# Performance work log

Hardware: AMD Instinct MI355X
Metric: run time of the kernel (lower is better)

Reference implementation:

```python
import jax, jax.numpy as jnp
import numpy as np
from jax import lax

M_SLOTS = 8192      # memory rows
N_DIM = 4096        # memory width; == FVS*FVS
FVS = 64            # function_vector_size
PLEN = 64           # max_program_length (== FVS so program->key fc is consistent)
CDIM = 256          # controller_dim
NIN, NOUT = 512, 512
STEPS = 8           # program length (number of program_i steps)
EPS = 1e-8


def setup_inputs() -> dict:
    key = jax.random.key(0)
    ks = jax.random.split(key, 15)
    s = 0.05
    stdev = 1.0 / np.sqrt(N_DIM + M_SLOTS)  # matches initalize_state uniform init
    return {
        "x": jax.random.normal(ks[0], (1, NIN), jnp.float32),
        "program": jax.random.normal(ks[1], (1, STEPS, PLEN), jnp.float32),
        "memory0": jax.random.uniform(ks[2], (M_SLOTS, N_DIM), jnp.float32, -stdev, stdev),
        "input_embedding": jax.random.normal(ks[3], (NIN, FVS), jnp.float32) * s,
        "output_embedding": jax.random.normal(ks[4], (FVS, NOUT), jnp.float32) * s,
        "Wc": jax.random.normal(ks[5], (CDIM, FVS + PLEN), jnp.float32) * s,
        "bc": jnp.zeros((CDIM,), jnp.float32),
        "Wk": jax.random.normal(ks[6], (N_DIM, CDIM), jnp.float32) * s,
        "bk": jnp.zeros((N_DIM,), jnp.float32),
        "We": jax.random.normal(ks[7], (N_DIM, CDIM), jnp.float32) * s,
        "be": jnp.zeros((N_DIM,), jnp.float32),
        "Wa": jax.random.normal(ks[8], (N_DIM, CDIM), jnp.float32) * s,
        "ba": jnp.zeros((N_DIM,), jnp.float32),
        "Wrk": jax.random.normal(ks[9], (N_DIM, PLEN), jnp.float32) * s,
        "brk": jnp.zeros((N_DIM,), jnp.float32),
    }


def _cosine_address(mem, k):
    # mem: [M, N], k: [N] -> softmax over M of cosine similarity (content addressing)
    sim = mem @ k  # [M]
    denom = jnp.sqrt(jnp.sum(mem * mem, axis=1)) * jnp.sqrt(jnp.sum(k * k)) + EPS
    return jax.nn.softmax(sim / denom)  # [M]


def _ntm_forward(x, program, memory0, input_embedding, output_embedding,
                 Wc, bc, Wk, bk, We, be, Wa, ba, Wrk, brk):
    X = x @ input_embedding  # [1, FVS]

    def step(carry, prog_t):
        Xc, mem = carry  # Xc: [1, FVS], mem: [M, N]
        # Controller: sigmoid(Linear(concat(X, program_i)))
        c = jax.nn.sigmoid(jnp.concatenate([Xc[0], prog_t]) @ Wc.T + bc)  # [CDIM]
        # Write head: key / erase / add from controller state, content addressing
        k = jnp.tanh(c @ Wk.T + bk)           # [N]
        e = jax.nn.sigmoid(c @ We.T + be)     # [N]
        a = jnp.tanh(c @ Wa.T + ba)           # [N]
        ww = _cosine_address(mem, k)          # [M]
        mem = mem * (1.0 - ww[:, None] * e[None, :]) + ww[:, None] * a[None, :]
        # Read head: key from program vector, content addressing on updated memory
        kr = jnp.tanh(prog_t @ Wrk.T + brk)   # [N]
        wr = _cosine_address(mem, kr)         # [M]
        read = wr @ mem                       # [N] == last_read
        # Executioner: X <- tanh(X @ last_read.view(FVS, FVS))
        Xn = jnp.tanh(Xc @ read.reshape(FVS, FVS))  # [1, FVS]
        return (Xn, mem), None

    (Xf, _memf), _ = lax.scan(step, (X, memory0), program[0])
    return Xf @ output_embedding  # [1, NOUT]


def reference(x, program, memory0, input_embedding, output_embedding,
              Wc, bc, Wk, bk, We, be, Wa, ba, Wrk, brk):
    return _ntm_forward(x, program, memory0, input_embedding, output_embedding,
                        Wc, bc, Wk, bk, We, be, Wa, ba, Wrk, brk)
```

## Files before the change

kernel.cpp:

```cpp
#include <hip/hip_runtime.h>
#include <hip/hip_fp16.h>
#include <math.h>

#define M_SLOTS 8192
#define N_DIM   4096
#define FVS     64
#define PLEN    64
#define CDIM    256
#define NIN     512
#define NOUT    512
#define STEPS   8
#define EPS_F   1e-8f

#define SROWS   16
#define NSB     (M_SLOTS / SROWS)
#define RROWS   32
#define NRB     (M_SLOTS / RROWS)


__device__ inline float wave_sum(float v) {
    for (int off = 32; off; off >>= 1) v += __shfl_down(v, off);
    return v;
}

__device__ inline float blk_sum_256(float v, float* sh) {
    v = wave_sum(v);
    int lane = threadIdx.x & 63, wid = threadIdx.x >> 6;
    if (lane == 0) sh[wid] = v;
    __syncthreads();
    float r = sh[0] + sh[1] + sh[2] + sh[3];
    __syncthreads();
    return r;
}

template<int CTRL>
__device__ inline float dppf(float x) {
    return __builtin_bit_cast(float, __builtin_amdgcn_update_dpp(
        0, __builtin_bit_cast(int, x), CTRL, 0xF, 0xF, true));
}

__device__ inline float group_reduce8_dpp(const float sv[8], int lane) {
    const bool b2 = (lane & 4) != 0;
    const bool b0 = (lane & 1) != 0;
    const bool b1 = (lane & 2) != 0;
    float a0 = (b2 ? sv[4] : sv[0]) + dppf<0x141>(b2 ? sv[0] : sv[4]);
    float a1 = (b2 ? sv[5] : sv[1]) + dppf<0x141>(b2 ? sv[1] : sv[5]);
    float a2 = (b2 ? sv[6] : sv[2]) + dppf<0x141>(b2 ? sv[2] : sv[6]);
    float a3 = (b2 ? sv[7] : sv[3]) + dppf<0x141>(b2 ? sv[3] : sv[7]);
    float c0 = (b0 ? a2 : a0) + dppf<0xB1>(b0 ? a0 : a2);
    float c1 = (b0 ? a3 : a1) + dppf<0xB1>(b0 ? a1 : a3);
    return (b1 ? c1 : c0) + dppf<0x4E>(b1 ? c0 : c1);
}

__device__ inline float4 ldh4(const unsigned short* __restrict__ base, size_t idx4) {
    ushort4 u = ((const ushort4*)base)[idx4];
    return make_float4(__half2float(__ushort_as_half(u.x)),
                       __half2float(__ushort_as_half(u.y)),
                       __half2float(__ushort_as_half(u.z)),
                       __half2float(__ushort_as_half(u.w)));
}

template<int NUP>
__device__ inline void ld_ww8(const float* __restrict__ wwT, int m, float wv[8]) {
    const float4* p = (const float4*)(wwT + (size_t)m * 8);
    if (NUP > 0) {
        float4 w0 = p[0];
        wv[0] = w0.x; wv[1] = w0.y; wv[2] = w0.z; wv[3] = w0.w;
    }
    if (NUP > 4) {
        float4 w1 = p[1];
        wv[4] = w1.x; wv[5] = w1.y; wv[6] = w1.z; wv[7] = w1.w;
    }
}


__global__ __launch_bounds__(256) void k_convert(const float* __restrict__ src,
                                                 unsigned short* __restrict__ dst) {
    size_t i = (size_t)blockIdx.x * 256 + threadIdx.x;
    float4 v = ((const float4*)src)[i];
    ushort4 o;
    o.x = __half_as_ushort(__float2half_rn(v.x));
    o.y = __half_as_ushort(__float2half_rn(v.y));
    o.z = __half_as_ushort(__float2half_rn(v.z));
    o.w = __half_as_ushort(__float2half_rn(v.w));
    ((ushort4*)dst)[i] = o;
}

__global__ void k_init_ctrl(const float* __restrict__ x, const float* __restrict__ emb,
                            const float* __restrict__ prog0,
                            const float* __restrict__ Wc, const float* __restrict__ bc,
                            float* __restrict__ X, float* __restrict__ c) {
    __shared__ float in[FVS + PLEN];
    int tid = threadIdx.x;
    if (tid < FVS) {
        float acc = 0.f;
        for (int i = 0; i < NIN; ++i) acc += x[i] * emb[i * FVS + tid];
        X[tid] = acc;
        in[tid] = acc;
    } else if (tid < FVS + PLEN) {
        in[tid] = prog0[tid - FVS];
    }
    __syncthreads();
    float acc = bc[tid];
    const float* wrow = Wc + tid * (FVS + PLEN);
    #pragma unroll 8
    for (int i = 0; i < FVS + PLEN; ++i) acc += wrow[i] * in[i];
    c[tid] = 1.f / (1.f + expf(-acc));
}

__device__ inline void keys_row(int gw, float4 cv, int lane, const float* __restrict__ prog,
                                const float* __restrict__ Wk, const float* __restrict__ bk,
                                const float* __restrict__ We, const float* __restrict__ be,
                                const float* __restrict__ Wa, const float* __restrict__ ba,
                                const float* __restrict__ Wrk, const float* __restrict__ brk,
                                float* __restrict__ k, float* __restrict__ e,
                                float* __restrict__ a, float* __restrict__ kr,
                                float* __restrict__ ekr, float* __restrict__ ea,
                                float* __restrict__ e2) {
    float4 wv;
    wv = ((const float4*)(Wk + (size_t)gw * CDIM))[lane];
    float sK = wv.x*cv.x + wv.y*cv.y + wv.z*cv.z + wv.w*cv.w;
    wv = ((const float4*)(We + (size_t)gw * CDIM))[lane];
    float sE = wv.x*cv.x + wv.y*cv.y + wv.z*cv.z + wv.w*cv.w;
    wv = ((const float4*)(Wa + (size_t)gw * CDIM))[lane];
    float sA = wv.x*cv.x + wv.y*cv.y + wv.z*cv.z + wv.w*cv.w;
    float sR = Wrk[(size_t)gw * PLEN + lane] * prog[lane];
    sK = wave_sum(sK); sE = wave_sum(sE); sA = wave_sum(sA); sR = wave_sum(sR);
    if (lane == 0) {
        float ev  = 1.f / (1.f + expf(-(sE + be[gw])));
        float av  = tanhf(sA + ba[gw]);
        float krv = tanhf(sR + brk[gw]);
        k[gw]   = tanhf(sK + bk[gw]);
        e[gw]   = ev;
        a[gw]   = av;
        kr[gw]  = krv;
        ekr[gw] = ev * krv;
        ea[gw]  = ev * av;
        e2[gw]  = ev * ev;
    }
}

__global__ __launch_bounds__(256) void k_keys4(
        const float* __restrict__ c, const float* __restrict__ prog,
        const float* __restrict__ Wk, const float* __restrict__ bk,
        const float* __restrict__ We, const float* __restrict__ be,
        const float* __restrict__ Wa, const float* __restrict__ ba,
        const float* __restrict__ Wrk, const float* __restrict__ brk,
        float* __restrict__ k, float* __restrict__ e,
        float* __restrict__ a, float* __restrict__ kr,
        float* __restrict__ ekr, float* __restrict__ ea, float* __restrict__ e2) {
    int lane = threadIdx.x & 63, wid = threadIdx.x >> 6;
    const float4 cv = ((const float4*)c)[lane];
    for (int gw = blockIdx.x * 4 + wid; gw < 4096; gw += 2048)
        keys_row(gw, cv, lane, prog, Wk, bk, We, be, Wa, ba, Wrk, brk,
                 k, e, a, kr, ekr, ea, e2);
}


template<int NUP>
__global__ __launch_bounds__(256) void k_stats(
        const unsigned short* __restrict__ mem0h,
        const float* __restrict__ ehist, const float* __restrict__ ahist,
        const float* __restrict__ wwT,
        const float* __restrict__ kc, const float* __restrict__ krc,
        const float* __restrict__ ekrc, const float* __restrict__ eac,
        const float* __restrict__ e2c,
        float* __restrict__ stat4) {
    const int tid  = threadIdx.x;
    const int cc   = blockIdx.x;
    const int rb   = blockIdx.y;
    const int col4 = cc * 256 + tid;
    const int lane = tid & 63, wid = tid >> 6;
    const int HN   = (NUP > 0) ? NUP : 1;
    float4 eh[HN], ah[HN];
    #pragma unroll
    for (int s = 0; s < NUP; ++s) {
        eh[s] = ((const float4*)(ehist + (size_t)s * N_DIM))[col4];
        ah[s] = ((const float4*)(ahist + (size_t)s * N_DIM))[col4];
    }
    const float4 kk  = ((const float4*)kc)[col4];
    const float4 rr  = ((const float4*)krc)[col4];
    const float4 fkr = ((const float4*)ekrc)[col4];
    const float4 fea = ((const float4*)eac)[col4];
    const float4 fe2 = ((const float4*)e2c)[col4];
    const float4 ce  = ((const float4*)(ehist + (size_t)NUP * N_DIM))[col4];
    const float4 ca  = ((const float4*)(ahist + (size_t)NUP * N_DIM))[col4];

    __shared__ float shc[4][SROWS][64];

    const int stl = (lane & 4) + 2 * (lane & 1) + ((lane & 2) >> 1);

    #pragma unroll
    for (int r = 0; r < SROWS; ++r) {
        const int m = rb * SROWS + r;
        float4 v = ldh4(mem0h, (size_t)m * (N_DIM / 4) + col4);
        float wv[8];
        ld_ww8<NUP>(wwT, m, wv);
        #pragma unroll
        for (int s = 0; s < NUP; ++s) {
            const float w = wv[s];
            v.x = v.x * (1.f - w * eh[s].x) + w * ah[s].x;
            v.y = v.y * (1.f - w * eh[s].y) + w * ah[s].y;
            v.z = v.z * (1.f - w * eh[s].z) + w * ah[s].z;
            v.w = v.w * (1.f - w * eh[s].w) + w * ah[s].w;
        }
        float sv[8] = {0.f, 0.f, 0.f, 0.f, 0.f, 0.f, 0.f, 0.f};
        #define ACC1(vv,kc_,rc_,ekr_,ac_,ea_,ec_,e2_) { \
            float _v = vv; float _v2 = _v * _v; \
            sv[0] += _v * kc_;  sv[1] += _v * rc_;  sv[2] += _v * ekr_; \
            sv[3] += _v * ac_;  sv[4] += _v * ea_;  sv[5] += _v * _v; \
            sv[6] += _v2 * ec_; sv[7] += _v2 * e2_; }
        ACC1(v.x, kk.x, rr.x, fkr.x, ca.x, fea.x, ce.x, fe2.x)
        ACC1(v.y, kk.y, rr.y, fkr.y, ca.y, fea.y, ce.y, fe2.y)
        ACC1(v.z, kk.z, rr.z, fkr.z, ca.z, fea.z, ce.z, fe2.z)
        ACC1(v.w, kk.w, rr.w, fkr.w, ca.w, fea.w, ce.w, fe2.w)
        #undef ACC1
        float g = group_reduce8_dpp(sv, lane);
        shc[wid][r][(lane & 56) + stl] = g;
    }
    __syncthreads();
    if (tid < SROWS * 8) {
        const int r = tid >> 3, st = tid & 7;
        float tot = 0.f;
        #pragma unroll
        for (int w = 0; w < 4; ++w)
            #pragma unroll
            for (int g2 = 0; g2 < 8; ++g2)
                tot += shc[w][r][g2 * 8 + st];
        stat4[(size_t)(cc * 8 + st) * M_SLOTS + rb * SROWS + r] = tot;
    }
}

#define ST4(st, m) (stat4[(size_t)(st) * M_SLOTS + (m)] \
                  + stat4[(size_t)((st) + 8) * M_SLOTS + (m)] \
                  + stat4[(size_t)((st) + 16) * M_SLOTS + (m)] \
                  + stat4[(size_t)((st) + 24) * M_SLOTS + (m)])

__global__ __launch_bounds__(256) void k_addrA(
        const float* __restrict__ kc, const float* __restrict__ stat4,
        float* __restrict__ exp1, float* __restrict__ n2sav,
        float* __restrict__ psum1) {
    __shared__ float sh4[4];
    const int tid = threadIdx.x, b = blockIdx.x;
    float a0 = 0.f;
    for (int i = tid; i < N_DIM; i += 256) { float kv = kc[i]; a0 += kv * kv; }
    float d0 = blk_sum_256(a0, sh4);
    float knorm = sqrtf(d0);
    float ls = 0.f;
    #pragma unroll
    for (int j = 0; j < 2; ++j) {
        int m = b * 512 + j * 256 + tid;
        float sim = ST4(0, m);
        float n2  = ST4(5, m);
        float v = sim / (sqrtf(n2) * knorm + EPS_F);
        float ex = expf(v);
        exp1[m] = ex;
        n2sav[m] = n2;
        ls += ex;
    }
    float tot = blk_sum_256(ls, sh4);
    if (tid == 0) psum1[b] = tot;
}

template<int NHIST>
__global__ __launch_bounds__(256) void k_read(
        const unsigned short* __restrict__ mem0h,
        const float* __restrict__ ehist, const float* __restrict__ ahist,
        float* __restrict__ wwT,
        const float* __restrict__ krc,
        const float* __restrict__ exp1, const float* __restrict__ n2sav,
        const float* __restrict__ psum1, const float* __restrict__ stat4,
        float* __restrict__ psum2,
        float* __restrict__ partial) {
    const int tid  = threadIdx.x;
    const int cc   = blockIdx.x;
    const int rb   = blockIdx.y;
    const int col4 = cc * 256 + tid;

    __shared__ float sh4[4];
    __shared__ float w1s[RROWS];
    __shared__ float wrs[RROWS];

    const float* ac = ahist + (size_t)NHIST * N_DIM;
    float a1 = 0.f, a2 = 0.f, a3 = 0.f;
    for (int i = tid; i < N_DIM; i += 256) {
        float rv = krc[i], av = ac[i];
        a1 += rv * rv; a2 += av * rv; a3 += av * av;
    }
    float d1 = blk_sum_256(a1, sh4);
    float d2 = blk_sum_256(a2, sh4);
    float d3 = blk_sum_256(a3, sh4);
    float krnorm = sqrtf(d1);

    float s1 = 0.f;
    #pragma unroll
    for (int i = 0; i < 16; ++i) s1 += psum1[i];
    const float inv1 = 1.f / s1;

    if (tid < RROWS) {
        const int m = rb * RROWS + tid;
        float w1 = exp1[m] * inv1;
        w1s[tid] = w1;
        float skr  = ST4(1, m);
        float sekr = ST4(2, m);
        float sa_  = ST4(3, m);
        float sea_ = ST4(4, m);
        float qe_  = ST4(6, m);
        float qe2_ = ST4(7, m);
        float sim2 = skr - w1 * sekr + w1 * d2;
        float n2n  = n2sav[m] - 2.f*w1*qe_ + w1*w1*qe2_
                   + 2.f*w1*sa_ - 2.f*w1*w1*sea_ + w1*w1*d3;
        float v2 = sim2 / (sqrtf(n2n) * krnorm + EPS_F);
        wrs[tid] = expf(v2);
        if (cc == 0) wwT[(size_t)m * 8 + NHIST] = w1;
    }
    __syncthreads();
    if (cc == 0 && tid == 0) {
        float s = 0.f;
        #pragma unroll
        for (int r = 0; r < RROWS; ++r) s += wrs[r];
        psum2[rb] = s;
    }

    const int HN = (NHIST > 0) ? NHIST : 1;
    float4 eh[HN], ah[HN];
    #pragma unroll
    for (int s = 0; s < NHIST; ++s) {
        eh[s] = ((const float4*)(ehist + (size_t)s * N_DIM))[col4];
        ah[s] = ((const float4*)(ahist + (size_t)s * N_DIM))[col4];
    }
    const float4 ce = ((const float4*)(ehist + (size_t)NHIST * N_DIM))[col4];
    const float4 ca = ((const float4*)(ahist + (size_t)NHIST * N_DIM))[col4];

    float4 acc = make_float4(0.f, 0.f, 0.f, 0.f);
    for (int r = 0; r < RROWS; ++r) {
        const int m = rb * RROWS + r;
        float4 v = ldh4(mem0h, (size_t)m * (N_DIM / 4) + col4);
        float wv[8];
        ld_ww8<NHIST>(wwT, m, wv);
        #pragma unroll
        for (int s = 0; s < NHIST; ++s) {
            const float w = wv[s];
            v.x = v.x * (1.f - w * eh[s].x) + w * ah[s].x;
            v.y = v.y * (1.f - w * eh[s].y) + w * ah[s].y;
            v.z = v.z * (1.f - w * eh[s].z) + w * ah[s].z;
            v.w = v.w * (1.f - w * eh[s].w) + w * ah[s].w;
        }
        {
            const float w1 = w1s[r];
            v.x = v.x * (1.f - w1 * ce.x) + w1 * ca.x;
            v.y = v.y * (1.f - w1 * ce.y) + w1 * ca.y;
            v.z = v.z * (1.f - w1 * ce.z) + w1 * ca.z;
            v.w = v.w * (1.f - w1 * ce.w) + w1 * ca.w;
        }
        const float w2 = wrs[r];
        acc.x += w2 * v.x; acc.y += w2 * v.y; acc.z += w2 * v.z; acc.w += w2 * v.w;
    }
    ((float4*)partial)[(size_t)rb * (N_DIM / 4) + col4] = acc;
}

__global__ void k_read_reduce(const float* __restrict__ partial,
                              const float* __restrict__ psum2,
                              float* __restrict__ red) {
    __shared__ float sh4[4];
    __shared__ float gsh[4][64];
    float p = psum2[threadIdx.x];
    float tot = blk_sum_256(p, sh4);
    float inv2 = 1.f / tot;
    int l = threadIdx.x & 63;
    int q = threadIdx.x >> 6;
    int c = blockIdx.x * 64 + l;
    float acc = 0.f;
    #pragma unroll 8
    for (int r = q * (NRB / 4); r < (q + 1) * (NRB / 4); ++r)
        acc += partial[(size_t)r * N_DIM + c];
    gsh[q][l] = acc;
    __syncthreads();
    if (threadIdx.x < 64)
        red[blockIdx.x * 64 + threadIdx.x] = inv2 *
            (gsh[0][threadIdx.x] + gsh[1][threadIdx.x] +
             gsh[2][threadIdx.x] + gsh[3][threadIdx.x]);
}

__global__ __launch_bounds__(256) void k_exec_keys(
        const float* __restrict__ Xold, float* __restrict__ Xnew,
        const float* __restrict__ red, const float* __restrict__ prog_next,
        const float* __restrict__ Wc, const float* __restrict__ bc,
        const float* __restrict__ Wk, const float* __restrict__ bk,
        const float* __restrict__ We, const float* __restrict__ be,
        const float* __restrict__ Wa, const float* __restrict__ ba,
        const float* __restrict__ Wrk, const float* __restrict__ brk,
        float* __restrict__ k, float* __restrict__ e,
        float* __restrict__ a, float* __restrict__ kr,
        float* __restrict__ ekr, float* __restrict__ ea, float* __restrict__ e2) {
    __shared__ float xo[FVS];
    __shared__ float xs[FVS];
    __shared__ float cc[CDIM];
    int tid = threadIdx.x, lane = tid & 63, wid = tid >> 6;
    if (tid < FVS) xo[tid] = Xold[tid];
    __syncthreads();
    if (tid < FVS) {
        float acc = 0.f;
        #pragma unroll
        for (int i = 0; i < FVS; ++i) acc += xo[i] * red[i * FVS + tid];
        float xn = tanhf(acc);
        xs[tid] = xn;
        if (blockIdx.x == 0) Xnew[tid] = xn;
    }
    __syncthreads();
    {
        float acc = bc[tid];
        const float* wrow = Wc + tid * (FVS + PLEN);
        #pragma unroll
        for (int i = 0; i < FVS; ++i) acc += wrow[i] * xs[i];
        #pragma unroll
        for (int i = 0; i < PLEN; ++i) acc += wrow[FVS + i] * prog_next[i];
        cc[tid] = 1.f / (1.f + expf(-acc));
    }
    __syncthreads();
    const float4 cv = ((const float4*)cc)[lane];
    for (int gw = blockIdx.x * 4 + wid; gw < 4096; gw += 2048)
        keys_row(gw, cv, lane, prog_next, Wk, bk, We, be, Wa, ba, Wrk, brk,
                 k, e, a, kr, ekr, ea, e2);
}

__global__ void k_final(const float* __restrict__ Xold, const float* __restrict__ red,
                        const float* __restrict__ out_emb, float* __restrict__ out) {
    __shared__ float xo[FVS];
    __shared__ float xs[FVS];
    int tid = threadIdx.x;
    if (tid < FVS) xo[tid] = Xold[tid];
    __syncthreads();
    if (tid < FVS) {
        float acc = 0.f;
        #pragma unroll
        for (int i = 0; i < FVS; ++i) acc += xo[i] * red[i * FVS + tid];
        xs[tid] = tanhf(acc);
    }
    __syncthreads();
    for (int col = tid; col < NOUT; col += 256) {
        float acc = 0.f;
        #pragma unroll
        for (int i = 0; i < FVS; ++i) acc += xs[i] * out_emb[i * NOUT + col];
        out[col] = acc;
    }
}


extern "C" void kernel_launch(void* const* d_in, const int* in_sizes, int n_in,
                              void* d_out, int out_size, void* d_ws, size_t ws_size,
                              hipStream_t stream) {
    const float* x        = (const float*)d_in[0];
    const float* program  = (const float*)d_in[1];
    const float* memory0  = (const float*)d_in[2];
    const float* in_emb   = (const float*)d_in[3];
    const float* out_emb  = (const float*)d_in[4];
    const float* Wc       = (const float*)d_in[5];
    const float* bc       = (const float*)d_in[6];
    const float* Wk       = (const float*)d_in[7];
    const float* bk       = (const float*)d_in[8];
    const float* We       = (const float*)d_in[9];
    const float* be       = (const float*)d_in[10];
    const float* Wa       = (const float*)d_in[11];
    const float* ba       = (const float*)d_in[12];
    const float* Wrk      = (const float*)d_in[13];
    const float* brk      = (const float*)d_in[14];
    float* out = (float*)d_out;

    float* ws = (float*)d_ws;
    size_t off = 0;
    unsigned short* mem0h = (unsigned short*)(ws + off);
    off += (size_t)M_SLOTS * N_DIM / 2;
    float* ehist   = ws + off; off += (size_t)STEPS * N_DIM;
    float* ahist   = ws + off; off += (size_t)STEPS * N_DIM;
    float* wwT     = ws + off; off += (size_t)M_SLOTS * 8;
    float* kcur    = ws + off; off += N_DIM;
    float* krcur   = ws + off; off += N_DIM;
    float* ekrcur  = ws + off; off += N_DIM;
    float* eacur   = ws + off; off += N_DIM;
    float* e2cur   = ws + off; off += N_DIM;
    float* stat4   = ws + off; off += (size_t)32 * M_SLOTS;
    float* partial = ws + off; off += (size_t)NRB * N_DIM;
    float* exp1    = ws + off; off += M_SLOTS;
    float* n2sav   = ws + off; off += M_SLOTS;
    float* psum1   = ws + off; off += 16;
    float* psum2   = ws + off; off += NRB;
    float* red     = ws + off; off += N_DIM;
    float* Xb0     = ws + off; off += FVS;
    float* Xb1     = ws + off; off += FVS;
    float* c       = ws + off; off += CDIM;

    k_convert<<<(M_SLOTS * (N_DIM / 4)) / 256, 256, 0, stream>>>(memory0, mem0h);
    k_init_ctrl<<<1, 256, 0, stream>>>(x, in_emb, program, Wc, bc, Xb0, c);
    k_keys4<<<512, 256, 0, stream>>>(c, program, Wk, bk, We, be, Wa, ba, Wrk, brk,
                                     kcur, ehist, ahist, krcur, ekrcur, eacur, e2cur);

    const dim3 sgrid(4, NSB), rgrid(4, NRB);

    for (int t = 0; t < STEPS; ++t) {
        switch (t) {
            case 0: k_stats<0><<<sgrid, 256, 0, stream>>>(mem0h, ehist, ahist, wwT,
                        kcur, krcur, ekrcur, eacur, e2cur, stat4); break;
            case 1: k_stats<1><<<sgrid, 256, 0, stream>>>(mem0h, ehist, ahist, wwT,
                        kcur, krcur, ekrcur, eacur, e2cur, stat4); break;
            case 2: k_stats<2><<<sgrid, 256, 0, stream>>>(mem0h, ehist, ahist, wwT,
                        kcur, krcur, ekrcur, eacur, e2cur, stat4); break;
            case 3: k_stats<3><<<sgrid, 256, 0, stream>>>(mem0h, ehist, ahist, wwT,
                        kcur, krcur, ekrcur, eacur, e2cur, stat4); break;
            case 4: k_stats<4><<<sgrid, 256, 0, stream>>>(mem0h, ehist, ahist, wwT,
                        kcur, krcur, ekrcur, eacur, e2cur, stat4); break;
            case 5: k_stats<5><<<sgrid, 256, 0, stream>>>(mem0h, ehist, ahist, wwT,
                        kcur, krcur, ekrcur, eacur, e2cur, stat4); break;
            case 6: k_stats<6><<<sgrid, 256, 0, stream>>>(mem0h, ehist, ahist, wwT,
                        kcur, krcur, ekrcur, eacur, e2cur, stat4); break;
            case 7: k_stats<7><<<sgrid, 256, 0, stream>>>(mem0h, ehist, ahist, wwT,
                        kcur, krcur, ekrcur, eacur, e2cur, stat4); break;
        }

        k_addrA<<<16, 256, 0, stream>>>(kcur, stat4, exp1, n2sav, psum1);

        switch (t) {
            case 0: k_read<0><<<rgrid, 256, 0, stream>>>(mem0h, ehist, ahist, wwT,
                        krcur, exp1, n2sav, psum1, stat4, psum2, partial); break;
            case 1: k_read<1><<<rgrid, 256, 0, stream>>>(mem0h, ehist, ahist, wwT,
                        krcur, exp1, n2sav, psum1, stat4, psum2, partial); break;
            case 2: k_read<2><<<rgrid, 256, 0, stream>>>(mem0h, ehist, ahist, wwT,
                        krcur, exp1, n2sav, psum1, stat4, psum2, partial); break;
            case 3: k_read<3><<<rgrid, 256, 0, stream>>>(mem0h, ehist, ahist, wwT,
                        krcur, exp1, n2sav, psum1, stat4, psum2, partial); break;
            case 4: k_read<4><<<rgrid, 256, 0, stream>>>(mem0h, ehist, ahist, wwT,
                        krcur, exp1, n2sav, psum1, stat4, psum2, partial); break;
            case 5: k_read<5><<<rgrid, 256, 0, stream>>>(mem0h, ehist, ahist, wwT,
                        krcur, exp1, n2sav, psum1, stat4, psum2, partial); break;
            case 6: k_read<6><<<rgrid, 256, 0, stream>>>(mem0h, ehist, ahist, wwT,
                        krcur, exp1, n2sav, psum1, stat4, psum2, partial); break;
            case 7: k_read<7><<<rgrid, 256, 0, stream>>>(mem0h, ehist, ahist, wwT,
                        krcur, exp1, n2sav, psum1, stat4, psum2, partial); break;
        }

        k_read_reduce<<<64, 256, 0, stream>>>(partial, psum2, red);

        const float* Xcur = (t & 1) ? Xb1 : Xb0;
        float*       Xnxt = (t & 1) ? Xb0 : Xb1;
        if (t < STEPS - 1) {
            k_exec_keys<<<512, 256, 0, stream>>>(
                Xcur, Xnxt, red, program + (t + 1) * PLEN,
                Wc, bc, Wk, bk, We, be, Wa, ba, Wrk, brk,
                kcur, ehist + (size_t)(t + 1) * N_DIM,
                ahist + (size_t)(t + 1) * N_DIM, krcur, ekrcur, eacur, e2cur);
        } else {
            k_final<<<1, 256, 0, stream>>>(Xcur, red, out_emb, out);
        }
    }
}
```

Measured before the change: 690.1 us.

## Remap k_stats so each lane owns a memory row and loops over columns

Rewrites the stats kernel so that each lane accumulates all eight statistics for one memory row across a 128-column strip. The per-column vectors are then wave-uniform broadcast loads, which replaces the DPP cross-lane reduction with a small shared-memory reduction over 8 waves. Blocks grow to 512 threads, covering 64 rows by 1024 columns. The cost is that the fp16 memory loads within a wave now stride across 64 different rows, so they are no longer coalesced, and it relies on L1/L2 to reuse cache lines across loop iterations.

```diff
diff --git a/kernel.cpp b/kernel.cpp
--- a/kernel.cpp
+++ b/kernel.cpp
@@ -12,8 +12,6 @@
 #define STEPS   8
 #define EPS_F   1e-8f
 
-#define SROWS   16
-#define NSB     (M_SLOTS / SROWS)
 #define RROWS   32
 #define NRB     (M_SLOTS / RROWS)
 
@@ -31,25 +29,6 @@
     float r = sh[0] + sh[1] + sh[2] + sh[3];
     __syncthreads();
     return r;
-}
-
-template<int CTRL>
-__device__ inline float dppf(float x) {
-    return __builtin_bit_cast(float, __builtin_amdgcn_update_dpp(
-        0, __builtin_bit_cast(int, x), CTRL, 0xF, 0xF, true));
-}
-
-__device__ inline float group_reduce8_dpp(const float sv[8], int lane) {
-    const bool b2 = (lane & 4) != 0;
-    const bool b0 = (lane & 1) != 0;
-    const bool b1 = (lane & 2) != 0;
-    float a0 = (b2 ? sv[4] : sv[0]) + dppf<0x141>(b2 ? sv[0] : sv[4]);
-    float a1 = (b2 ? sv[5] : sv[1]) + dppf<0x141>(b2 ? sv[1] : sv[5]);
-    float a2 = (b2 ? sv[6] : sv[2]) + dppf<0x141>(b2 ? sv[2] : sv[6]);
-    float a3 = (b2 ? sv[7] : sv[3]) + dppf<0x141>(b2 ? sv[3] : sv[7]);
-    float c0 = (b0 ? a2 : a0) + dppf<0xB1>(b0 ? a0 : a2);
-    float c1 = (b0 ? a3 : a1) + dppf<0xB1>(b0 ? a1 : a3);
-    return (b1 ? c1 : c0) + dppf<0x4E>(b1 ? c0 : c1);
 }
 
 __device__ inline float4 ldh4(const unsigned short* __restrict__ base, size_t idx4) {
@@ -158,7 +137,7 @@
 
 
 template<int NUP>
-__global__ __launch_bounds__(256) void k_stats(
+__global__ __launch_bounds__(512) void k_stats(
         const unsigned short* __restrict__ mem0h,
         const float* __restrict__ ehist, const float* __restrict__ ahist,
         const float* __restrict__ wwT,
@@ -169,65 +148,60 @@
     const int tid  = threadIdx.x;
     const int cc   = blockIdx.x;
     const int rb   = blockIdx.y;
-    const int col4 = cc * 256 + tid;
-    const int lane = tid & 63, wid = tid >> 6;
-    const int HN   = (NUP > 0) ? NUP : 1;
-    float4 eh[HN], ah[HN];
+    const int lane = tid & 63;
+    const int w    = tid >> 6;
+    const int row  = rb * 64 + lane;
+
+    float wv[8];
+    ld_ww8<NUP>(wwT, row, wv);
+
+    const int j0base = cc * 1024 + w * 128;
+    const size_t rowbase = (size_t)row * N_DIM;
+
+    float sv[8] = {0.f, 0.f, 0.f, 0.f, 0.f, 0.f, 0.f, 0.f};
+
+    for (int it = 0; it < 32; ++it) {
+        const int j0 = j0base + it * 4;
+        float4 vv = ldh4(mem0h, (rowbase + j0) >> 2);
+        #pragma unroll
+        for (int s = 0; s < NUP; ++s) {
+            const float4 eh = *(const float4*)(ehist + (size_t)s * N_DIM + j0);
+            const float4 ah = *(const float4*)(ahist + (size_t)s * N_DIM + j0);
+            const float wc = wv[s];
+            vv.x = vv.x * (1.f - wc * eh.x) + wc * ah.x;
+            vv.y = vv.y * (1.f - wc * eh.y) + wc * ah.y;
+            vv.z = vv.z * (1.f - wc * eh.z) + wc * ah.z;
+            vv.w = vv.w * (1.f - wc * eh.w) + wc * ah.w;
+        }
+        const float4 kk  = *(const float4*)(kc + j0);
+        const float4 rr  = *(const float4*)(krc + j0);
+        const float4 fkr = *(const float4*)(ekrc + j0);
+        const float4 ca  = *(const float4*)(ahist + (size_t)NUP * N_DIM + j0);
+        const float4 fea = *(const float4*)(eac + j0);
+        const float4 ce  = *(const float4*)(ehist + (size_t)NUP * N_DIM + j0);
+        const float4 fe2 = *(const float4*)(e2c + j0);
+        #define ACC1(vvc,kc_,rc_,ekr_,ac_,ea_,ec_,e2_) { \
+            float _v = vvc; float _v2 = _v * _v; \
+            sv[0] += _v * kc_;  sv[1] += _v * rc_;  sv[2] += _v * ekr_; \
+            sv[3] += _v * ac_;  sv[4] += _v * ea_;  sv[5] += _v2; \
+            sv[6] += _v2 * ec_; sv[7] += _v2 * e2_; }
+        ACC1(vv.x, kk.x, rr.x, fkr.x, ca.x, fea.x, ce.x, fe2.x)
+        ACC1(vv.y, kk.y, rr.y, fkr.y, ca.y, fea.y, ce.y, fe2.y)
+        ACC1(vv.z, kk.z, rr.z, fkr.z, ca.z, fea.z, ce.z, fe2.z)
+        ACC1(vv.w, kk.w, rr.w, fkr.w, ca.w, fea.w, ce.w, fe2.w)
+        #undef ACC1
+    }
+
+    __shared__ float shc[8][64][8];
     #pragma unroll
-    for (int s = 0; s < NUP; ++s) {
-        eh[s] = ((const float4*)(ehist + (size_t)s * N_DIM))[col4];
-        ah[s] = ((const float4*)(ahist + (size_t)s * N_DIM))[col4];
-    }
-    const float4 kk  = ((const float4*)kc)[col4];
-    const float4 rr  = ((const float4*)krc)[col4];
-    const float4 fkr = ((const float4*)ekrc)[col4];
-    const float4 fea = ((const float4*)eac)[col4];
-    const float4 fe2 = ((const float4*)e2c)[col4];
-    const float4 ce  = ((const float4*)(ehist + (size_t)NUP * N_DIM))[col4];
-    const float4 ca  = ((const float4*)(ahist + (size_t)NUP * N_DIM))[col4];
-
-    __shared__ float shc[4][SROWS][64];
-
-    const int stl = (lane & 4) + 2 * (lane & 1) + ((lane & 2) >> 1);
-
-    #pragma unroll
-    for (int r = 0; r < SROWS; ++r) {
-        const int m = rb * SROWS + r;
-        float4 v = ldh4(mem0h, (size_t)m * (N_DIM / 4) + col4);
-        float wv[8];
-        ld_ww8<NUP>(wwT, m, wv);
-        #pragma unroll
-        for (int s = 0; s < NUP; ++s) {
-            const float w = wv[s];
-            v.x = v.x * (1.f - w * eh[s].x) + w * ah[s].x;
-            v.y = v.y * (1.f - w * eh[s].y) + w * ah[s].y;
-            v.z = v.z * (1.f - w * eh[s].z) + w * ah[s].z;
-            v.w = v.w * (1.f - w * eh[s].w) + w * ah[s].w;
-        }
-        float sv[8] = {0.f, 0.f, 0.f, 0.f, 0.f, 0.f, 0.f, 0.f};
-        #define ACC1(vv,kc_,rc_,ekr_,ac_,ea_,ec_,e2_) { \
-            float _v = vv; float _v2 = _v * _v; \
-            sv[0] += _v * kc_;  sv[1] += _v * rc_;  sv[2] += _v * ekr_; \
-            sv[3] += _v * ac_;  sv[4] += _v * ea_;  sv[5] += _v * _v; \
-            sv[6] += _v2 * ec_; sv[7] += _v2 * e2_; }
-        ACC1(v.x, kk.x, rr.x, fkr.x, ca.x, fea.x, ce.x, fe2.x)
-        ACC1(v.y, kk.y, rr.y, fkr.y, ca.y, fea.y, ce.y, fe2.y)
-        ACC1(v.z, kk.z, rr.z, fkr.z, ca.z, fea.z, ce.z, fe2.z)
-        ACC1(v.w, kk.w, rr.w, fkr.w, ca.w, fea.w, ce.w, fe2.w)
-        #undef ACC1
-        float g = group_reduce8_dpp(sv, lane);
-        shc[wid][r][(lane & 56) + stl] = g;
-    }
-    __syncthreads();
-    if (tid < SROWS * 8) {
+    for (int st = 0; st < 8; ++st) shc[w][lane][st] = sv[st];
+    __syncthreads();
+    {
         const int r = tid >> 3, st = tid & 7;
         float tot = 0.f;
         #pragma unroll
-        for (int w = 0; w < 4; ++w)
-            #pragma unroll
-            for (int g2 = 0; g2 < 8; ++g2)
-                tot += shc[w][r][g2 * 8 + st];
-        stat4[(size_t)(cc * 8 + st) * M_SLOTS + rb * SROWS + r] = tot;
+        for (int q = 0; q < 8; ++q) tot += shc[q][r][st];
+        stat4[(size_t)(cc * 8 + st) * M_SLOTS + rb * 64 + r] = tot;
     }
 }
 
@@ -495,25 +469,25 @@
     k_keys4<<<512, 256, 0, stream>>>(c, program, Wk, bk, We, be, Wa, ba, Wrk, brk,
                                      kcur, ehist, ahist, krcur, ekrcur, eacur, e2cur);
 
-    const dim3 sgrid(4, NSB), rgrid(4, NRB);
+    const dim3 sgrid(4, M_SLOTS / 64), rgrid(4, NRB);
 
     for (int t = 0; t < STEPS; ++t) {
         switch (t) {
-            case 0: k_stats<0><<<sgrid, 256, 0, stream>>>(mem0h, ehist, ahist, wwT,
-                        kcur, krcur, ekrcur, eacur, e2cur, stat4); break;
-            case 1: k_stats<1><<<sgrid, 256, 0, stream>>>(mem0h, ehist, ahist, wwT,
-                        kcur, krcur, ekrcur, eacur, e2cur, stat4); break;
-            case 2: k_stats<2><<<sgrid, 256, 0, stream>>>(mem0h, ehist, ahist, wwT,
-                        kcur, krcur, ekrcur, eacur, e2cur, stat4); break;
-            case 3: k_stats<3><<<sgrid, 256, 0, stream>>>(mem0h, ehist, ahist, wwT,
-                        kcur, krcur, ekrcur, eacur, e2cur, stat4); break;
-            case 4: k_stats<4><<<sgrid, 256, 0, stream>>>(mem0h, ehist, ahist, wwT,
-                        kcur, krcur, ekrcur, eacur, e2cur, stat4); break;
-            case 5: k_stats<5><<<sgrid, 256, 0, stream>>>(mem0h, ehist, ahist, wwT,
-                        kcur, krcur, ekrcur, eacur, e2cur, stat4); break;
-            case 6: k_stats<6><<<sgrid, 256, 0, stream>>>(mem0h, ehist, ahist, wwT,
-                        kcur, krcur, ekrcur, eacur, e2cur, stat4); break;
-            case 7: k_stats<7><<<sgrid, 256, 0, stream>>>(mem0h, ehist, ahist, wwT,
+            case 0: k_stats<0><<<sgrid, 512, 0, stream>>>(mem0h, ehist, ahist, wwT,
+                        kcur, krcur, ekrcur, eacur, e2cur, stat4); break;
+            case 1: k_stats<1><<<sgrid, 512, 0, stream>>>(mem0h, ehist, ahist, wwT,
+                        kcur, krcur, ekrcur, eacur, e2cur, stat4); break;
+            case 2: k_stats<2><<<sgrid, 512, 0, stream>>>(mem0h, ehist, ahist, wwT,
+                        kcur, krcur, ekrcur, eacur, e2cur, stat4); break;
+            case 3: k_stats<3><<<sgrid, 512, 0, stream>>>(mem0h, ehist, ahist, wwT,
+                        kcur, krcur, ekrcur, eacur, e2cur, stat4); break;
+            case 4: k_stats<4><<<sgrid, 512, 0, stream>>>(mem0h, ehist, ahist, wwT,
+                        kcur, krcur, ekrcur, eacur, e2cur, stat4); break;
+            case 5: k_stats<5><<<sgrid, 512, 0, stream>>>(mem0h, ehist, ahist, wwT,
+                        kcur, krcur, ekrcur, eacur, e2cur, stat4); break;
+            case 6: k_stats<6><<<sgrid, 512, 0, stream>>>(mem0h, ehist, ahist, wwT,
+                        kcur, krcur, ekrcur, eacur, e2cur, stat4); break;
+            case 7: k_stats<7><<<sgrid, 512, 0, stream>>>(mem0h, ehist, ahist, wwT,
                         kcur, krcur, ekrcur, eacur, e2cur, stat4); break;
         }
 
```

Measured after the change: 1.745 ms. 2.53x slower.
